# Kernel optimization log

Hardware: AMD Instinct MI355X
Metric: run time of the kernel (lower is better)

## Reference

```python
import jax, jax.numpy as jnp
import numpy as np

M1, M2, M3 = 12, 12, 8
WIDTH = 32


def _spectral_conv(v, wr, wi):
    # v: [B, C, X, Y, T]; wr/wi: [4, Ci, Co, M1, M2, M3]
    B, C, X, Y, T = v.shape
    vft = jnp.fft.rfftn(v, axes=(-3, -2, -1))  # [B,C,X,Y,T//2+1] complex
    w = wr.astype(jnp.complex64) + 1j * wi.astype(jnp.complex64)
    mul = lambda blk, ww: jnp.einsum('bixyz,ioxyz->boxyz', blk, ww)
    out = jnp.zeros((B, wr.shape[2], X, Y, T // 2 + 1), dtype=vft.dtype)
    out = out.at[:, :, :M1, :M2, :M3].set(mul(vft[:, :, :M1, :M2, :M3], w[0]))
    out = out.at[:, :, -M1:, :M2, :M3].set(mul(vft[:, :, -M1:, :M2, :M3], w[1]))
    out = out.at[:, :, :M1, -M2:, :M3].set(mul(vft[:, :, :M1, -M2:, :M3], w[2]))
    out = out.at[:, :, -M1:, -M2:, :M3].set(mul(vft[:, :, -M1:, -M2:, :M3], w[3]))
    return jnp.fft.irfftn(out, s=(X, Y, T), axes=(-3, -2, -1))


def _conv1x1(v, w, b):
    # v: [B,C,X,Y,T]; w: [Co,Ci]; b: [Co]
    return jnp.einsum('bixyz,oi->boxyz', v, w) + b[None, :, None, None, None]


def setup_inputs() -> dict:
    key = jax.random.key(0)
    ks = jax.random.split(key, 24)
    B, X, Y, T = 8, 64, 64, 40
    W = WIDTH
    scale = 1.0 / (W * W)
    d = {}
    d['h'] = jax.random.normal(ks[0], (B, X, Y, T, 2), dtype=jnp.float32)
    d['x'] = jax.random.normal(ks[1], (B, X, Y, T, 3), dtype=jnp.float32)
    d['fc0_w'] = jax.random.normal(ks[2], (5, W), dtype=jnp.float32) * 0.3
    d['fc0_b'] = jnp.zeros((W,), dtype=jnp.float32)
    for i, name in enumerate(['sc0', 'sc1', 'sc3']):
        d[name + '_wr'] = scale * jax.random.uniform(ks[3 + 2 * i], (4, W, W, M1, M2, M3), dtype=jnp.float32)
        d[name + '_wi'] = scale * jax.random.uniform(ks[4 + 2 * i], (4, W, W, M1, M2, M3), dtype=jnp.float32)
    for i, name in enumerate(['w0', 'w1', 'w3']):
        d[name + '_w'] = jax.random.normal(ks[9 + 2 * i], (W, W), dtype=jnp.float32) * (1.0 / np.sqrt(W))
        d[name + '_b'] = jnp.zeros((W,), dtype=jnp.float32)
    d['fc1_w'] = jax.random.normal(ks[15], (W, 64), dtype=jnp.float32) * (1.0 / np.sqrt(W))
    d['fc1_b'] = jnp.zeros((64,), dtype=jnp.float32)
    d['fc2_w'] = jax.random.normal(ks[16], (64, 2), dtype=jnp.float32) * 0.125
    d['fc2_b'] = jnp.zeros((2,), dtype=jnp.float32)
    return d


def reference(h, x, fc0_w, fc0_b, sc0_wr, sc0_wi, sc1_wr, sc1_wi, sc3_wr, sc3_wi,
              w0_w, w0_b, w1_w, w1_b, w3_w, w3_b, fc1_w, fc1_b, fc2_w, fc2_b):
    v = jnp.concatenate((h, x), axis=-1)                 # [B,X,Y,T,5]
    v = v @ fc0_w + fc0_b                                # lift to width
    v = jnp.transpose(v, (0, 4, 1, 2, 3))                # [B,W,X,Y,T]
    v = jax.nn.gelu(_spectral_conv(v, sc0_wr, sc0_wi) + _conv1x1(v, w0_w, w0_b), approximate=False)
    v = jax.nn.gelu(_spectral_conv(v, sc1_wr, sc1_wi) + _conv1x1(v, w1_w, w1_b), approximate=False)
    v = _spectral_conv(v, sc3_wr, sc3_wi) + _conv1x1(v, w3_w, w3_b)
    v = jnp.transpose(v, (0, 2, 3, 4, 1))                # [B,X,Y,T,W]
    v = jax.nn.gelu(v @ fc1_w + fc1_b, approximate=False)
    return v @ fc2_w + fc2_b                             # [B,X,Y,T,2]
```

## Files before the change

kernel.cpp:

```cpp
#include <hip/hip_runtime.h>
#include <math.h>

#define BATCH 8
#define WID   32
#define NX    64
#define NY    64
#define NT    40
#define M1C   12
#define KT    8
#define KXC   24
#define KYC   24
#define NXY   (NX*NY)
#define NXYT  (NXY*NT)
#define NP    (BATCH*NXYT)

#define TWO_PI 6.283185307179586f

static __device__ __forceinline__ float gelu_f(float v){
  return 0.5f*v*(1.0f + erff(v*0.7071067811865476f));
}

static __device__ __forceinline__ void barrier_lds(){
  asm volatile("s_waitcnt lgkmcnt(0)\n\ts_barrier" ::: "memory");
}


__global__ __launch_bounds__(256) void k_fc0(const float* __restrict__ h, const float* __restrict__ x,
                                             const float* __restrict__ w, const float* __restrict__ b,
                                             float* __restrict__ V){
  __shared__ float sw[160], sb[32];
  int tid=threadIdx.x;
  if(tid<160) sw[tid]=w[tid];
  if(tid<32)  sb[tid]=b[tid];
  __syncthreads();
  int pl = tid>>3, q = tid&7;
  int p = blockIdx.x*32 + pl;
  float i0=h[(size_t)p*2], i1=h[(size_t)p*2+1];
  float i2=x[(size_t)p*3], i3=x[(size_t)p*3+1], i4=x[(size_t)p*3+2];
  int c0=q*4;
  float4 o;
  float* po=(float*)&o;
  #pragma unroll
  for(int u=0;u<4;u++){
    int c=c0+u;
    po[u] = sb[c] + i0*sw[c] + i1*sw[32+c] + i2*sw[64+c] + i3*sw[96+c] + i4*sw[128+c];
  }
  ((float4*)V)[(size_t)p*8 + q] = o;
}

__global__ __launch_bounds__(256) void k_fwd_ty(const float* __restrict__ V, float2* __restrict__ F2){
  __shared__ __align__(16) unsigned char smem[26624];
  float*  vt    = (float*)smem;
  float2* twy   = (float2*)(smem + 20480);
  float2* f2out = (float2*)smem;
  int tid = threadIdx.x;
  int b = blockIdx.x >> 7, x = (blockIdx.x >> 1) & 63, kyh = blockIdx.x & 1;
  int c = tid & 31, k = tid >> 5;
  for(int i=tid;i<12*NY;i+=256){
    int kyl=i>>6, y=i&63;
    int ky = kyh*12 + kyl;
    int f = ky<M1C ? ky : ky+40;
    float ang = -TWO_PI*(float)((f*y)%NY)/(float)NY;
    twy[i] = make_float2(cosf(ang), sinf(ang));
  }
  float2 twr[20];
  #pragma unroll
  for(int t=0;t<20;t++){
    float ang = -TWO_PI*(float)((k*t)%NT)/(float)NT;
    twr[t] = make_float2(cosf(ang), sinf(ang));
  }
  float sgn = (k&1) ? -1.0f : 1.0f;
  float2 acc[12];
  #pragma unroll
  for(int q=0;q<12;q++) acc[q]=make_float2(0.f,0.f);
  const float4* src = (const float4*)(V + (size_t)(b*NX+x)*(NY*NT*WID));
  for(int g=0; g<16; g++){
    __syncthreads();
    #pragma unroll
    for(int r=0;r<5;r++) ((float4*)vt)[r*256+tid] = src[g*1280 + r*256 + tid];
    __syncthreads();
    #pragma unroll
    for(int yl=0; yl<4; yl+=2){
      float sr0=0.f, si0=0.f, sr1=0.f, si1=0.f;
      const float* vp0 = vt + yl*1280 + c;
      const float* vp1 = vp0 + 1280;
      #pragma unroll
      for(int t=0;t<20;t++){
        float2 w = twr[t];
        float u0 = fmaf(sgn, vp0[(t+20)*32], vp0[t*32]);
        float u1 = fmaf(sgn, vp1[(t+20)*32], vp1[t*32]);
        sr0 += u0*w.x; si0 += u0*w.y;
        sr1 += u1*w.x; si1 += u1*w.y;
      }
      int y = g*4 + yl;
      #pragma unroll
      for(int q=0;q<12;q++){
        float4 wy = *(const float4*)&twy[q*NY + y];
        acc[q].x += sr0*wy.x - si0*wy.y + sr1*wy.z - si1*wy.w;
        acc[q].y += sr0*wy.y + si0*wy.x + sr1*wy.w + si1*wy.z;
      }
    }
  }
  __syncthreads();
  #pragma unroll
  for(int q=0;q<12;q++) f2out[c*97 + q*8 + k] = acc[q];
  __syncthreads();
  for(int i=tid;i<WID*96;i+=256){
    int cc=i/96, e=i-cc*96;
    F2[((size_t)(b*WID+cc)*NX + x)*(KYC*KT) + kyh*96 + e] = f2out[cc*97 + e];
  }
}

__global__ __launch_bounds__(256) void k_fwd_x(const float2* __restrict__ F2, float2* __restrict__ F3){
  __shared__ float2 tile[NX*KT];
  __shared__ float2 twi[KXC*65];
  int tid=threadIdx.x;
  int bc = blockIdx.x / KYC;
  int ky = blockIdx.x - bc*KYC;
  for(int i=tid;i<NX*KT;i+=256){
    int xx=i/KT, kt=i-xx*KT;
    tile[i] = F2[((size_t)bc*NX + xx)*(KYC*KT) + ky*KT + kt];
  }
  for(int i=tid;i<KXC*NX;i+=256){
    int kx=i/NX, xx=i-kx*NX;
    int f = kx<M1C ? kx : kx+40;
    float ang = -TWO_PI*(float)((f*xx)%NX)/(float)NX;
    twi[kx*65+xx] = make_float2(cosf(ang), sinf(ang));
  }
  __syncthreads();
  for(int item=tid; item<KXC*KT; item+=256){
    int kx=item/KT, kt=item-kx*KT;
    float sr=0.f, si=0.f;
    #pragma unroll 8
    for(int xx=0;xx<NX;xx++){
      float2 a = tile[xx*KT+kt];
      float2 w = twi[kx*65+xx];
      sr += a.x*w.x - a.y*w.y;
      si += a.x*w.y + a.y*w.x;
    }
    F3[(size_t)bc*(KXC*KYC*KT) + kx*(KYC*KT) + ky*KT + kt] = make_float2(sr,si);
  }
}

__global__ __launch_bounds__(256) void k_mix(const float2* __restrict__ F3, const float* __restrict__ wr,
                                             const float* __restrict__ wi, float2* __restrict__ F4){
  __shared__ float2 f3s[BATCH*WID*KT];
  int tid = threadIdx.x;
  int kx = blockIdx.x / KYC, ky = blockIdx.x - kx*KYC;
  int mode0 = blockIdx.x * KT;
  int xp = (kx>=M1C), yp = (ky>=M1C);
  int m1 = kx - M1C*xp, m2 = ky - M1C*yp;
  int blk = xp + 2*yp;
  for(int i=tid;i<1024;i+=256){
    int row=i>>2, q=i&3;
    ((float4*)f3s)[row*4+q] = ((const float4*)(F3 + (size_t)row*4608 + mode0))[q];
  }
  int o = tid>>3, kt = tid&7;
  size_t wbase = (size_t)blk*1179648 + (size_t)o*1152 + m1*96 + m2*8 + kt;
  float wre[WID], wim[WID];
  #pragma unroll
  for(int i=0;i<WID;i++){
    wre[i] = wr[wbase + (size_t)i*36864];
    wim[i] = wi[wbase + (size_t)i*36864];
  }
  __syncthreads();
  #pragma unroll
  for(int b=0;b<BATCH;b++){
    float ar=0.f, ai=0.f;
    #pragma unroll
    for(int i=0;i<WID;i++){
      float2 a = f3s[(b*WID+i)*KT + kt];
      ar += a.x*wre[i] - a.y*wim[i];
      ai += a.x*wim[i] + a.y*wre[i];
    }
    F4[(size_t)(b*WID+o)*4608 + mode0 + kt] = make_float2(ar,ai);
  }
}

__global__ __launch_bounds__(256) void k_inv_x(const float2* __restrict__ F4, float2* __restrict__ F2){
  __shared__ float2 tile[KXC*KT];
  __shared__ float2 twi[NX*25];
  int tid=threadIdx.x;
  int bc = blockIdx.x / KYC, ky = blockIdx.x - (blockIdx.x/KYC)*KYC;
  for(int i=tid;i<KXC*KT;i+=256){
    int kx=i/KT, kt=i-kx*KT;
    tile[i] = F4[(size_t)bc*4608 + kx*(KYC*KT) + ky*KT + kt];
  }
  for(int i=tid;i<NX*KXC;i+=256){
    int xx=i/KXC, kx=i-xx*KXC;
    int f = kx<M1C ? kx : kx+40;
    float ang = TWO_PI*(float)((f*xx)%NX)/(float)NX;
    twi[xx*25+kx] = make_float2(cosf(ang)*(1.0f/64.0f), sinf(ang)*(1.0f/64.0f));
  }
  __syncthreads();
  for(int item=tid; item<NX*KT; item+=256){
    int xx=item/KT, kt=item-xx*KT;
    float sr=0.f, si=0.f;
    #pragma unroll 8
    for(int kx=0;kx<KXC;kx++){
      float2 a = tile[kx*KT+kt];
      float2 w = twi[xx*25+kx];
      sr += a.x*w.x - a.y*w.y;
      si += a.x*w.y + a.y*w.x;
    }
    F2[((size_t)bc*NX + xx)*(KYC*KT) + ky*KT + kt] = make_float2(sr,si);
  }
}

template<bool GELU>
__global__ __launch_bounds__(256) void k_conv(const float2* __restrict__ F2, const float* __restrict__ wcv,
                                              const float* __restrict__ bcv, float* __restrict__ V){
  __shared__ __align__(16) unsigned char smem[34816];
  float*  vtA  = (float*)smem;
  float*  vtB  = (float*)(smem+10240);
  float2* ftc0 = (float2*)(smem+20480);
  float2* ftc1 = (float2*)(smem+24576);
  float2* twy  = (float2*)(smem+28672);
  float2* f2h  = (float2*)smem;

  int tid=threadIdx.x;
  int b  = blockIdx.x >> 7;
  int x  = (blockIdx.x >> 1) & 63;
  int y0 = (blockIdx.x & 1) * 32;
  int cid = tid & 31, ktid = tid >> 5;
  int oid = tid & 31, tg  = tid >> 5;

  float2 fr[KYC];
  #pragma unroll
  for(int half=0; half<2; half++){
    for(int i=tid;i<1536;i+=256){
      int cc=i/96, q=i-cc*96;
      ((float4*)f2h)[i] = *((const float4*)(F2 + ((size_t)(b*WID + half*16 + cc)*NX + x)*(KYC*KT)) + q);
    }
    __syncthreads();
    if((cid>>4) == half){
      const float2* fp = f2h + (cid&15)*192 + ktid;
      #pragma unroll
      for(int ky=0;ky<KYC;ky++) fr[ky] = fp[ky*8];
    }
    __syncthreads();
  }
  {
    float ts = (ktid==0 ? 1.0f : 2.0f) * (1.0f/(float)NT);
    #pragma unroll
    for(int ky=0;ky<KYC;ky++){ fr[ky].x *= ts; fr[ky].y *= ts; }
  }
  float wreg[WID];
  #pragma unroll
  for(int cc=0;cc<WID;cc++) wreg[cc] = wcv[oid*WID + cc];
  float breg = bcv[oid];
  float2 twtg[KT];
  #pragma unroll
  for(int k=0;k<KT;k++){
    float ang = 0.78539816339744831f*(float)((k*tg)&7);
    twtg[k] = make_float2(cosf(ang), sinf(ang));
  }
  for(int i=tid;i<32*KYC;i+=256){
    int yy=i/KYC, ky=i-yy*KYC;
    int f = ky<M1C ? ky : ky+40;
    float ang = TWO_PI*(float)((f*(y0+yy))%NY)/(float)NY;
    twy[i] = make_float2(cosf(ang)*(1.0f/64.0f), sinf(ang)*(1.0f/64.0f));
  }
  float* plane = V + (size_t)((b*NX+x)*NY + y0)*(NT*WID);
  const float4* gp = (const float4*)plane;
  bool has3 = tid < 128;
  {
    float4 p0 = gp[tid], p1 = gp[256+tid];
    float4 p2 = has3 ? gp[512+tid] : make_float4(0,0,0,0);
    ((float4*)vtA)[tid] = p0;
    ((float4*)vtA)[256+tid] = p1;
    if(has3) ((float4*)vtA)[512+tid] = p2;
  }
  float4 rA = gp[640+tid], rB = gp[640+256+tid];
  float4 rC = has3 ? gp[640+512+tid] : make_float4(0,0,0,0);
  __syncthreads();

  constexpr float CJ[KT][5] = {
    {1.f, 1.f,          1.f,          1.f,          1.f         },
    {1.f, 0.98768834f,  0.95105652f,  0.89100652f,  0.80901699f },
    {1.f, 0.95105652f,  0.80901699f,  0.58778525f,  0.30901699f },
    {1.f, 0.89100652f,  0.58778525f,  0.15643447f, -0.30901699f },
    {1.f, 0.80901699f,  0.30901699f, -0.30901699f, -0.80901699f },
    {1.f, 0.70710678f,  0.f,         -0.70710678f, -1.f         },
    {1.f, 0.58778525f, -0.30901699f, -0.95105652f, -0.80901699f },
    {1.f, 0.45399050f, -0.58778525f, -0.98768834f, -0.30901699f },
  };
  constexpr float SJ[KT][5] = {
    {0.f, 0.f,          0.f,          0.f,          0.f         },
    {0.f, 0.15643447f,  0.30901699f,  0.45399050f,  0.58778525f },
    {0.f, 0.30901699f,  0.58778525f,  0.80901699f,  0.95105652f },
    {0.f, 0.45399050f,  0.80901699f,  0.98768834f,  0.95105652f },
    {0.f, 0.58778525f,  0.95105652f,  0.95105652f,  0.58778525f },
    {0.f, 0.70710678f,  1.f,          0.70710678f,  0.f         },
    {0.f, 0.80901699f,  0.95105652f,  0.30901699f, -0.58778525f },
    {0.f, 0.89100652f,  0.80901699f, -0.15643447f, -0.95105652f },
  };

  #pragma unroll 1
  for(int it=0; it<16; ++it){
    float*  vcur = (it&1) ? vtB  : vtA;
    float*  vnxt = (it&1) ? vtA  : vtB;
    float2* fcur = (it&1) ? ftc1 : ftc0;
    int yl = it*2;
    {
      const float2* tw0 = twy + (size_t)yl*KYC;
      const float2* tw1 = tw0 + KYC;
      float sr0=0.f, si0=0.f, sr1=0.f, si1=0.f;
      #pragma unroll
      for(int ky=0;ky<KYC;ky+=2){
        float2 a  = fr[ky];
        float2 b2 = fr[ky+1];
        float4 w0 = *(const float4*)&tw0[ky];
        float4 w1 = *(const float4*)&tw1[ky];
        sr0 += a.x*w0.x - a.y*w0.y + b2.x*w0.z - b2.y*w0.w;
        si0 += a.x*w0.y + a.y*w0.x + b2.x*w0.w + b2.y*w0.z;
        sr1 += a.x*w1.x - a.y*w1.y + b2.x*w1.z - b2.y*w1.w;
        si1 += a.x*w1.y + a.y*w1.x + b2.x*w1.w + b2.y*w1.z;
      }
      fcur[      ktid*32 + cid] = make_float2(sr0,si0);
      fcur[256 + ktid*32 + cid] = make_float2(sr1,si1);
    }
    barrier_lds();
    if(it+1 < 16){
      ((float4*)vnxt)[tid] = rA;
      ((float4*)vnxt)[256+tid] = rB;
      if(has3) ((float4*)vnxt)[512+tid] = rC;
    }
    if(it+2 < 16){
      const float4* q = gp + (size_t)(it+2)*640;
      rA = q[tid]; rB = q[256+tid];
      if(has3) rC = q[512+tid];
    }
    #pragma unroll
    for(int yy=0; yy<2; yy++){
      const float2* fsrc = fcur + yy*256;
      const float*  vb   = vcur + yy*1280;
      float* outp = plane + (size_t)(yl+yy)*(NT*WID);
      float acc[5];
      #pragma unroll
      for(int j=0;j<5;j++) acc[j] = breg;
      #pragma unroll
      for(int k=0;k<KT;k++){
        float2 f = fsrc[k*32 + oid];
        float gx = f.x*twtg[k].x - f.y*twtg[k].y;
        float gy = f.x*twtg[k].y + f.y*twtg[k].x;
        #pragma unroll
        for(int j=0;j<5;j++) acc[j] += gx*CJ[k][j] - gy*SJ[k][j];
      }
      #pragma unroll
      for(int j=0;j<5;j++){
        int t = tg*5 + j;
        float a = acc[j];
        const float* vrow = vb + t*32;
        #pragma unroll
        for(int c4=0;c4<WID;c4+=4){
          float4 vv = *(const float4*)(vrow + c4);
          a += vv.x*wreg[c4] + vv.y*wreg[c4+1] + vv.z*wreg[c4+2] + vv.w*wreg[c4+3];
        }
        outp[t*32 + oid] = GELU ? gelu_f(a) : a;
      }
    }
  }
}

__global__ __launch_bounds__(256) void k_mlp(const float* __restrict__ V, const float* __restrict__ w1,
                                             const float* __restrict__ b1, const float* __restrict__ w2,
                                             const float* __restrict__ b2, float* __restrict__ out){
  __shared__ float sw1t[64*WID];
  __shared__ float sb1[64], sw2[128], sb2[2];
  int tid=threadIdx.x;
  for(int i=tid;i<64*WID;i+=256){ int j=i>>5, c=i&31; sw1t[i]=w1[c*64+j]; }
  if(tid<64) sb1[tid]=b1[tid];
  if(tid<128) sw2[tid]=w2[tid];
  if(tid<2) sb2[tid]=b2[tid];
  __syncthreads();
  size_t p0 = (size_t)blockIdx.x*1024 + (size_t)tid*4;
  float vv[128];
  const float4* vp = (const float4*)(V + p0*WID);
  #pragma unroll
  for(int q=0;q<32;q++) *((float4*)(vv+4*q)) = vp[q];
  float oa[8];
  #pragma unroll
  for(int pt=0;pt<4;pt++){ oa[2*pt]=sb2[0]; oa[2*pt+1]=sb2[1]; }
  #pragma unroll 4
  for(int j=0;j<64;j++){
    float a0=sb1[j], a1=a0, a2=a0, a3=a0;
    const float* wrow = sw1t + j*WID;
    #pragma unroll
    for(int c4=0;c4<WID;c4+=4){
      float4 w = *(const float4*)(wrow + c4);
      a0 += vv[     c4]*w.x + vv[     c4+1]*w.y + vv[     c4+2]*w.z + vv[     c4+3]*w.w;
      a1 += vv[32 + c4]*w.x + vv[32 + c4+1]*w.y + vv[32 + c4+2]*w.z + vv[32 + c4+3]*w.w;
      a2 += vv[64 + c4]*w.x + vv[64 + c4+1]*w.y + vv[64 + c4+2]*w.z + vv[64 + c4+3]*w.w;
      a3 += vv[96 + c4]*w.x + vv[96 + c4+1]*w.y + vv[96 + c4+2]*w.z + vv[96 + c4+3]*w.w;
    }
    a0=gelu_f(a0); a1=gelu_f(a1); a2=gelu_f(a2); a3=gelu_f(a3);
    float u0=sw2[2*j], u1=sw2[2*j+1];
    oa[0]+=a0*u0; oa[1]+=a0*u1; oa[2]+=a1*u0; oa[3]+=a1*u1;
    oa[4]+=a2*u0; oa[5]+=a2*u1; oa[6]+=a3*u0; oa[7]+=a3*u1;
  }
  float4* op = (float4*)(out + p0*2);
  op[0]=make_float4(oa[0],oa[1],oa[2],oa[3]);
  op[1]=make_float4(oa[4],oa[5],oa[6],oa[7]);
}

extern "C" void kernel_launch(void* const* d_in, const int* in_sizes, int n_in,
                              void* d_out, int out_size, void* d_ws, size_t ws_size,
                              hipStream_t stream){
  const float* h     = (const float*)d_in[0];
  const float* x     = (const float*)d_in[1];
  const float* fc0_w = (const float*)d_in[2];
  const float* fc0_b = (const float*)d_in[3];
  const float* scwr[3] = {(const float*)d_in[4], (const float*)d_in[6], (const float*)d_in[8]};
  const float* scwi[3] = {(const float*)d_in[5], (const float*)d_in[7], (const float*)d_in[9]};
  const float* cw[3]   = {(const float*)d_in[10], (const float*)d_in[12], (const float*)d_in[14]};
  const float* cb[3]   = {(const float*)d_in[11], (const float*)d_in[13], (const float*)d_in[15]};
  const float* fc1_w = (const float*)d_in[16];
  const float* fc1_b = (const float*)d_in[17];
  const float* fc2_w = (const float*)d_in[18];
  const float* fc2_b = (const float*)d_in[19];

  const size_t VSZ = (size_t)BATCH*WID*NXYT;
  float*  V  = (float*)d_ws;
  float2* F2 = (float2*)(V + VSZ);
  float2* F4 = F2 + (size_t)BATCH*WID*NX*KYC*KT;
  float2* F3 = (float2*)d_out;

  k_fc0<<<NP/32, 256, 0, stream>>>(h, x, fc0_w, fc0_b, V);
  for(int L=0; L<3; L++){
    k_fwd_ty<<<BATCH*NX*2, 256, 0, stream>>>(V, F2);
    k_fwd_x<<<(BATCH*WID)*KYC, 256, 0, stream>>>(F2, F3);
    k_mix<<<KXC*KYC, 256, 0, stream>>>(F3, scwr[L], scwi[L], F4);
    k_inv_x<<<(BATCH*WID)*KYC, 256, 0, stream>>>(F4, F2);
    if(L<2) k_conv<true ><<<BATCH*NX*2, 256, 0, stream>>>(F2, cw[L], cb[L], V);
    else    k_conv<false><<<BATCH*NX*2, 256, 0, stream>>>(F2, cw[L], cb[L], V);
  }
  k_mlp<<<NP/1024, 256, 0, stream>>>(V, fc1_w, fc1_b, fc2_w, fc2_b, (float*)d_out);
}
```

Baseline: 1.603 ms.

## Double-buffer forward T/Y DFT and compute all ky modes per block

Each block of the forward T/Y DFT kernel now computes all 24 ky modes instead of splitting them across two blocks, so each (b,x) slab of V is read once instead of twice. Tiles are double-buffered in LDS with register prefetch two steps ahead, and the even/odd time fold (a+b, a-b) is done once at store time, with a transposed padded layout that allows float2 LDS reads. The cost is half as many blocks (512), about twice the LDS per block, and more accumulator registers, which lowers occupancy.

```diff
diff --git a/kernel.cpp b/kernel.cpp
--- a/kernel.cpp
+++ b/kernel.cpp
@@ -49,16 +49,16 @@
 }
 
 __global__ __launch_bounds__(256) void k_fwd_ty(const float* __restrict__ V, float2* __restrict__ F2){
-  __shared__ __align__(16) unsigned char smem[26624];
-  float*  vt    = (float*)smem;
-  float2* twy   = (float2*)(smem + 20480);
+  __shared__ __align__(16) unsigned char smem[55296];
+  float*  vt0   = (float*)smem;
+  float*  vt1   = (float*)(smem+21504);
+  float2* twy   = (float2*)(smem+43008);
   float2* f2out = (float2*)smem;
   int tid = threadIdx.x;
-  int b = blockIdx.x >> 7, x = (blockIdx.x >> 1) & 63, kyh = blockIdx.x & 1;
+  int b = blockIdx.x >> 6, x = blockIdx.x & 63;
   int c = tid & 31, k = tid >> 5;
-  for(int i=tid;i<12*NY;i+=256){
-    int kyl=i>>6, y=i&63;
-    int ky = kyh*12 + kyl;
+  for(int i=tid;i<KYC*NY;i+=256){
+    int ky=i>>6, y=i&63;
     int f = ky<M1C ? ky : ky+40;
     float ang = -TWO_PI*(float)((f*y)%NY)/(float)NY;
     twy[i] = make_float2(cosf(ang), sinf(ang));
@@ -69,45 +69,112 @@
     float ang = -TWO_PI*(float)((k*t)%NT)/(float)NT;
     twr[t] = make_float2(cosf(ang), sinf(ang));
   }
-  float sgn = (k&1) ? -1.0f : 1.0f;
-  float2 acc[12];
-  #pragma unroll
-  for(int q=0;q<12;q++) acc[q]=make_float2(0.f,0.f);
+  int toff = (k&1)*20;
+  float2 acc[KYC];
+  #pragma unroll
+  for(int q=0;q<KYC;q++) acc[q]=make_float2(0.f,0.f);
   const float4* src = (const float4*)(V + (size_t)(b*NX+x)*(NY*NT*WID));
-  for(int g=0; g<16; g++){
-    __syncthreads();
-    #pragma unroll
-    for(int r=0;r<5;r++) ((float4*)vt)[r*256+tid] = src[g*1280 + r*256 + tid];
-    __syncthreads();
+
+  float4 pa[3], pb[3];
+  #pragma unroll
+  for(int i=0;i<3;i++){
+    int s = tid + i*256;
+    if(s<640){
+      int c4=s&7, t=(s>>3)%20, y=s/160;
+      pa[i] = src[y*320 + t*8 + c4];
+      pb[i] = src[y*320 + t*8 + c4 + 160];
+    }
+  }
+  #pragma unroll
+  for(int i=0;i<3;i++){
+    int s = tid + i*256;
+    if(s<640){
+      int c4=s&7, t=(s>>3)%20, y=s/160;
+      float* bse = vt0 + y*1344 + t;
+      #pragma unroll
+      for(int e=0;e<4;e++){
+        float av=((float*)&pa[i])[e], bv=((float*)&pb[i])[e];
+        bse[(4*c4+e)*42]      = av+bv;
+        bse[(4*c4+e)*42 + 20] = av-bv;
+      }
+    }
+  }
+  #pragma unroll
+  for(int i=0;i<3;i++){
+    int s = tid + i*256;
+    if(s<640){
+      int c4=s&7, t=(s>>3)%20, y=s/160;
+      pa[i] = src[1280 + y*320 + t*8 + c4];
+      pb[i] = src[1280 + y*320 + t*8 + c4 + 160];
+    }
+  }
+  __syncthreads();
+
+  #pragma unroll 1
+  for(int g=0; g<16; ++g){
+    const float* vb = (g&1) ? vt1 : vt0;
+    float* vn       = (g&1) ? vt0 : vt1;
+    if(g+1<16){
+      #pragma unroll
+      for(int i=0;i<3;i++){
+        int s = tid + i*256;
+        if(s<640){
+          int c4=s&7, t=(s>>3)%20, y=s/160;
+          float* bse = vn + y*1344 + t;
+          #pragma unroll
+          for(int e=0;e<4;e++){
+            float av=((float*)&pa[i])[e], bv=((float*)&pb[i])[e];
+            bse[(4*c4+e)*42]      = av+bv;
+            bse[(4*c4+e)*42 + 20] = av-bv;
+          }
+        }
+      }
+      if(g+2<16){
+        const float4* sg = src + (size_t)(g+2)*1280;
+        #pragma unroll
+        for(int i=0;i<3;i++){
+          int s = tid + i*256;
+          if(s<640){
+            int c4=s&7, t=(s>>3)%20, y=s/160;
+            pa[i] = sg[y*320 + t*8 + c4];
+            pb[i] = sg[y*320 + t*8 + c4 + 160];
+          }
+        }
+      }
+    }
     #pragma unroll
     for(int yl=0; yl<4; yl+=2){
-      float sr0=0.f, si0=0.f, sr1=0.f, si1=0.f;
-      const float* vp0 = vt + yl*1280 + c;
-      const float* vp1 = vp0 + 1280;
-      #pragma unroll
-      for(int t=0;t<20;t++){
-        float2 w = twr[t];
-        float u0 = fmaf(sgn, vp0[(t+20)*32], vp0[t*32]);
-        float u1 = fmaf(sgn, vp1[(t+20)*32], vp1[t*32]);
-        sr0 += u0*w.x; si0 += u0*w.y;
-        sr1 += u1*w.x; si1 += u1*w.y;
+      const float* vp0 = vb + yl*1344 + c*42 + toff;
+      const float* vp1 = vp0 + 1344;
+      float sr0=0.f,si0=0.f,sr1=0.f,si1=0.f;
+      #pragma unroll
+      for(int it=0; it<5; it++){
+        float2 a0 = *(const float2*)(vp0 + it*4);
+        float2 b0 = *(const float2*)(vp0 + it*4 + 2);
+        float2 a1 = *(const float2*)(vp1 + it*4);
+        float2 b1 = *(const float2*)(vp1 + it*4 + 2);
+        float2 w0=twr[it*4], w1=twr[it*4+1], w2=twr[it*4+2], w3=twr[it*4+3];
+        sr0 += a0.x*w0.x + a0.y*w1.x + b0.x*w2.x + b0.y*w3.x;
+        si0 += a0.x*w0.y + a0.y*w1.y + b0.x*w2.y + b0.y*w3.y;
+        sr1 += a1.x*w0.x + a1.y*w1.x + b1.x*w2.x + b1.y*w3.x;
+        si1 += a1.x*w0.y + a1.y*w1.y + b1.x*w2.y + b1.y*w3.y;
       }
       int y = g*4 + yl;
       #pragma unroll
-      for(int q=0;q<12;q++){
+      for(int q=0;q<KYC;q++){
         float4 wy = *(const float4*)&twy[q*NY + y];
         acc[q].x += sr0*wy.x - si0*wy.y + sr1*wy.z - si1*wy.w;
         acc[q].y += sr0*wy.y + si0*wy.x + sr1*wy.w + si1*wy.z;
       }
     }
-  }
-  __syncthreads();
-  #pragma unroll
-  for(int q=0;q<12;q++) f2out[c*97 + q*8 + k] = acc[q];
-  __syncthreads();
-  for(int i=tid;i<WID*96;i+=256){
-    int cc=i/96, e=i-cc*96;
-    F2[((size_t)(b*WID+cc)*NX + x)*(KYC*KT) + kyh*96 + e] = f2out[cc*97 + e];
+    barrier_lds();
+  }
+  #pragma unroll
+  for(int q=0;q<KYC;q++) f2out[c*193 + q*8 + k] = acc[q];
+  __syncthreads();
+  for(int i=tid;i<WID*KYC*KT;i+=256){
+    int cc=i/192, e=i-cc*192;
+    F2[((size_t)(b*WID+cc)*NX + x)*(KYC*KT) + e] = f2out[cc*193 + e];
   }
 }
 
@@ -428,7 +495,7 @@
 
   k_fc0<<<NP/32, 256, 0, stream>>>(h, x, fc0_w, fc0_b, V);
   for(int L=0; L<3; L++){
-    k_fwd_ty<<<BATCH*NX*2, 256, 0, stream>>>(V, F2);
+    k_fwd_ty<<<BATCH*NX, 256, 0, stream>>>(V, F2);
     k_fwd_x<<<(BATCH*WID)*KYC, 256, 0, stream>>>(F2, F3);
     k_mix<<<KXC*KYC, 256, 0, stream>>>(F3, scwr[L], scwi[L], F4);
     k_inv_x<<<(BATCH*WID)*KYC, 256, 0, stream>>>(F4, F2);
```

Result: faster. 1.402 ms (-12.5%).
